# Kernel optimization log

Hardware: AMD Instinct MI355X
Metric: run time of the kernel (lower is better)

Reference implementation:

```python
import jax, jax.numpy as jnp
import numpy as np

N_QUBITS = 8
N_LAYERS = 3
B = 32768
IN_F = 512
OUT_F = 512


def _apply_1q(state, G, q):
    # state: (B, 2,...,2) complex64; G: (2,2) shared or (B,2,2) per-sample gate
    s = jnp.moveaxis(state, 1 + q, -1)
    if G.ndim == 3:
        s = jnp.einsum('bij,...j->...i'.replace('...', 'b...').replace('b...ij', 'bij'), G, s) if False else jnp.einsum('bij,b...j->b...i', G, s)
    else:
        s = jnp.einsum('ij,b...j->b...i', G, s)
    return jnp.moveaxis(s, -1, 1 + q)


def _cnot(state, c, t):
    # flip target axis on the control=1 slice
    ca, ta = 1 + c, 1 + t
    s0 = jax.lax.index_in_dim(state, 0, ca, keepdims=True)
    s1 = jax.lax.index_in_dim(state, 1, ca, keepdims=True)
    s1 = jnp.flip(s1, axis=ta)
    return jnp.concatenate([s0, s1], axis=ca)


def _circuit(angles, qparams):
    # angles: (B, 8) RY embedding angles; qparams: (3, 8) RX layer angles
    b = angles.shape[0]
    state = jnp.zeros((b, 2 ** N_QUBITS), dtype=jnp.complex64).at[:, 0].set(1.0)
    state = state.reshape((b,) + (2,) * N_QUBITS)
    # RY(theta) = [[c, -s], [s, c]], per-sample angles
    half = 0.5 * angles
    c, s = jnp.cos(half), jnp.sin(half)
    for q in range(N_QUBITS):
        G = jnp.stack([jnp.stack([c[:, q], -s[:, q]], -1),
                       jnp.stack([s[:, q], c[:, q]], -1)], -2).astype(jnp.complex64)
        state = _apply_1q(state, G, q)
    # layers: RX(params[l,q]) on each wire, then ring of CNOTs
    hp = 0.5 * qparams
    cp, sp = jnp.cos(hp), jnp.sin(hp)
    for l in range(N_LAYERS):
        for q in range(N_QUBITS):
            # RX(theta) = [[c, -i s], [-i s, c]]
            G = jnp.stack([jnp.stack([cp[l, q] + 0j, -1j * sp[l, q]], -1),
                           jnp.stack([-1j * sp[l, q], cp[l, q] + 0j], -1)], -2).astype(jnp.complex64)
            state = _apply_1q(state, G, q)
        for i in range(N_QUBITS - 1):
            state = _cnot(state, i, i + 1)
        state = _cnot(state, N_QUBITS - 1, 0)
    # <Z_q> = P(bit_q=0) - P(bit_q=1)
    probs = jnp.real(state) ** 2 + jnp.imag(state) ** 2
    zs = []
    for q in range(N_QUBITS):
        p = jnp.moveaxis(probs, 1 + q, 1).reshape(b, 2, -1).sum(-1)
        zs.append(p[:, 0] - p[:, 1])
    return jnp.stack(zs, axis=1)  # (B, 8) float32


def setup_inputs() -> dict:
    key = jax.random.key(0)
    k = jax.random.split(key, 6)
    x = jax.random.normal(k[0], (B, IN_F), dtype=jnp.float32)
    fc_w = jax.random.normal(k[1], (N_QUBITS, IN_F), dtype=jnp.float32) / np.sqrt(IN_F)
    fc_b = jax.random.normal(k[2], (N_QUBITS,), dtype=jnp.float32) * 0.01
    qparams = jax.random.normal(k[3], (N_LAYERS, N_QUBITS), dtype=jnp.float32) * 0.1
    post_w = jax.random.normal(k[4], (OUT_F, N_QUBITS), dtype=jnp.float32) / np.sqrt(N_QUBITS)
    post_b = jax.random.normal(k[5], (OUT_F,), dtype=jnp.float32) * 0.01
    return {"x": x, "fc_w": fc_w, "fc_b": fc_b, "qparams": qparams,
            "post_w": post_w, "post_b": post_b}


def reference(x, fc_w, fc_b, qparams, post_w, post_b):
    xproj = x @ fc_w.T + fc_b            # (B, 8) angles
    z = _circuit(xproj, qparams)          # (B, 8) PauliZ expectations
    return z @ post_w.T + post_b          # (B, OUT_F)
```

## Files before the change

### kernel.cpp

```cpp
#include <hip/hip_runtime.h>

#define BLOCK 512
typedef float v2f __attribute__((ext_vector_type(2)));

__device__ __forceinline__ v2f pk_fma(v2f a, v2f b, v2f c) {
  v2f d;
  asm("v_pk_fma_f32 %0, %1, %2, %3" : "=v"(d) : "v"(a), "v"(b), "v"(c));
  return d;
}
__device__ __forceinline__ v2f pk_mul(v2f a, v2f b) {
  v2f d;
  asm("v_pk_mul_f32 %0, %1, %2" : "=v"(d) : "v"(a), "v"(b));
  return d;
}
__device__ __forceinline__ v2f pk_mul_swap(v2f s, v2f p) {
  v2f d;
  asm("v_pk_mul_f32 %0, %1, %2 op_sel:[0,1] op_sel_hi:[1,0]" : "=v"(d) : "v"(s), "v"(p));
  return d;
}

template<int CTRL>
__device__ __forceinline__ float dpp_f(float v) {
  return __int_as_float(__builtin_amdgcn_mov_dpp(__float_as_int(v), CTRL, 0xF, 0xF, true));
}
template<int MASK>
__device__ __forceinline__ float shx(float v) {
  if constexpr (MASK == 1)      return dpp_f<0xB1>(v);
  else if constexpr (MASK == 2) return dpp_f<0x4E>(v);
  else if constexpr (MASK == 8) return dpp_f<0x128>(v);
  else
    return __int_as_float(__builtin_amdgcn_ds_swizzle(__float_as_int(v), 0x101F));
}

__device__ __forceinline__ int gmap(int b) {
#pragma unroll
  for (int j = 0; j < 7; ++j) b ^= ((b >> (j + 1)) & 1) << j;
  b ^= (b & 1) << 7;
  return b;
}

__device__ __forceinline__ float dotK(const v2f* pp, const v2f* kcol) {
  v2f a0; a0.x = 0.f; a0.y = 0.f;
  v2f a1; a1.x = 0.f; a1.y = 0.f;
#pragma unroll
  for (int k = 0; k < 8; k += 2) {
    a0 = pk_fma(pp[k],     kcol[k * 16],       a0);
    a1 = pk_fma(pp[k + 1], kcol[(k + 1) * 16], a1);
  }
  return (a0.x + a1.x) + (a0.y + a1.y);
}

#define MQ_PACKED 0x99CC66B359AC5632ULL

__global__ __launch_bounds__(BLOCK, 4) void qcnn_kernel(
    const float* __restrict__ x,   const float* __restrict__ fcw,
    const float* __restrict__ fcb, const float* __restrict__ qp,
    const float* __restrict__ pw,  const float* __restrict__ pb,
    float* __restrict__ out)
{
  __shared__ float s_fcw[8 * 512];
  __shared__ float s_pwt[8 * 512];
  __shared__ float s_pb[512];
  __shared__ float s_beta[256];
  __shared__ v2f   s_K2[8][8][16];

  const int tid = threadIdx.x;

#pragma unroll
  for (int i = tid; i < 1024; i += BLOCK)
    ((float4*)s_fcw)[i] = ((const float4*)fcw)[i];
#pragma unroll
  for (int i = tid; i < 4096; i += BLOCK)
    s_pwt[i] = pw[(i & 511) * 8 + (i >> 9)];
  if (tid < 128) ((float4*)s_pb)[tid] = ((const float4*)pb)[tid];

  if (tid < 256) {
    const int c = tid;
    const int i1 = gmap(c);
    const int i2 = gmap(i1);
    float ang = 0.f;
#pragma unroll
    for (int q = 0; q < 8; ++q) {
      ang += (((c  >> q) & 1) ? 0.5f : -0.5f) * qp[q];
      ang += (((i1 >> q) & 1) ? 0.5f : -0.5f) * qp[8 + q];
      ang += (((i2 >> q) & 1) ? 0.5f : -0.5f) * qp[16 + q];
    }
    s_beta[c] = ang;
  }
  __syncthreads();

#pragma unroll
  for (int i = tid; i < 2048; i += BLOCK) {
    const int q = i >> 8, c = i & 255;
    const int m = (int)((MQ_PACKED >> (8 * q)) & 0xFF);
    const float kv = __cosf(s_beta[c ^ m] - s_beta[c]) * (1.0f / 256.0f);
    const int uu = c >> 4, rr = c & 15;
    ((float*)s_K2)[((q * 8 + (rr >> 1)) * 16 + uu) * 2 + (rr & 1)] = kv;
  }
  __syncthreads();

  const int wave = tid >> 6;
  const int lane = tid & 63;
  const int u = lane & 15;
  const int g = lane >> 4;

#pragma unroll 1
  for (int tile = 0; tile < 2; ++tile) {
    const int smp = blockIdx.x * 64 + tile * 32 + wave * 4 + g;

    const float* xrow = x + (size_t)smp * 512;
    v2f acc2[8];
#pragma unroll
    for (int q = 0; q < 8; ++q) { acc2[q].x = 0.f; acc2[q].y = 0.f; }
#pragma unroll
    for (int t = 0; t < 8; ++t) {
      const float4 xv = *(const float4*)(xrow + u * 4 + t * 64);
      v2f x01; x01.x = xv.x; x01.y = xv.y;
      v2f x23; x23.x = xv.z; x23.y = xv.w;
#pragma unroll
      for (int q = 0; q < 8; ++q) {
        const float4 wv = *(const float4*)(s_fcw + q * 512 + u * 4 + t * 64);
        v2f w01; w01.x = wv.x; w01.y = wv.y;
        v2f w23; w23.x = wv.z; w23.y = wv.w;
        acc2[q] = pk_fma(x01, w01, acc2[q]);
        acc2[q] = pk_fma(x23, w23, acc2[q]);
      }
    }
    float th[8];
#pragma unroll
    for (int q = 0; q < 8; ++q) {
      float a_ = acc2[q].x + acc2[q].y;
      a_ += shx<1>(a_); a_ += shx<2>(a_); a_ += shx<4>(a_); a_ += shx<8>(a_);
      th[q] = a_ + fcb[q];
    }

    float uf[8], vf[8];
#pragma unroll
    for (int q = 0; q < 8; ++q) {
      const float h = 0.5f * th[q];
      const float c_ = __cosf(h), s_ = __sinf(h);
      uf[q] = c_ + s_; vf[q] = c_ - s_;
    }
    v2f wr2[8];
    {
      v2f P01; P01.x = uf[0]; P01.y = vf[0];
      const float r12[4] = {uf[1] * uf[2], vf[1] * uf[2], uf[1] * vf[2], vf[1] * vf[2]};
#pragma unroll
      for (int k = 0; k < 8; ++k) {
        const float rest = r12[k & 3] * ((k & 4) ? vf[3] : uf[3]);
        v2f rr; rr.x = rest; rr.y = rest;
        wr2[k] = pk_mul(P01, rr);
      }
    }
    float wup[8];
    {
      const bool b4 = (u & 1), b5 = (u & 2), b6 = (u & 4), b7 = (u & 8);
      const float f4 = b4 ? vf[4] : uf[4], g4 = b4 ? uf[4] : vf[4];
      const float f5 = b5 ? vf[5] : uf[5], g5 = b5 ? uf[5] : vf[5];
      const float f6 = b6 ? vf[6] : uf[6], g6 = b6 ? uf[6] : vf[6];
      const float f7 = b7 ? vf[7] : uf[7], g7 = b7 ? uf[7] : vf[7];
      const float A0 = f4 * f5, A1 = g4 * f5, A2 = f4 * g5, A3 = g4 * g5;
      const float B0 = f6 * f7, B1 = g6 * f7, B2 = f6 * g7, B3 = g6 * g7;
      const float wu = A0 * B0;
      wup[0] = wu * (A3 * B0);
      wup[1] = wu * (A1 * B1);
      wup[2] = wu * (A2 * B2);
      wup[3] = wup[1];
      wup[4] = wu * (A3 * B2);
      wup[5] = wu * (A2 * B1);
      wup[6] = wu * (A0 * B3);
      wup[7] = wu * (A1 * B2);
    }

    float zp[8];
    {
      const v2f* kb = (const v2f*)s_K2 + u;
      v2f pp[8];
#pragma unroll
      for (int k = 0; k < 8; ++k) pp[k] = pk_mul(wr2[k], wr2[k ^ 1]);
      zp[0] = dotK(pp, kb + 0 * 128) * wup[0];
#pragma unroll
      for (int k = 0; k < 8; ++k) pp[k] = pk_mul_swap(wr2[k], wr2[k ^ 1]);
      zp[4] = dotK(pp, kb + 4 * 128) * wup[4];
#pragma unroll
      for (int k = 0; k < 8; ++k) pp[k] = pk_mul(wr2[k], wr2[k ^ 3]);
      zp[1] = dotK(pp, kb + 1 * 128) * wup[1];
      zp[5] = dotK(pp, kb + 5 * 128) * wup[5];
#pragma unroll
      for (int k = 0; k < 8; ++k) pp[k] = pk_mul(wr2[k], wr2[k ^ 6]);
      zp[2] = dotK(pp, kb + 2 * 128) * wup[2];
      zp[6] = dotK(pp, kb + 6 * 128) * wup[6];
#pragma unroll
      for (int k = 0; k < 8; ++k) pp[k] = pk_mul_swap(wr2[k], wr2[k ^ 4]);
      zp[3] = dotK(pp, kb + 3 * 128) * wup[3];
      zp[7] = dotK(pp, kb + 7 * 128) * wup[7];
    }
#pragma unroll
    for (int q = 0; q < 8; ++q) zp[q] += shx<1>(zp[q]);
#pragma unroll
    for (int q = 0; q < 8; ++q) zp[q] += shx<2>(zp[q]);
#pragma unroll
    for (int q = 0; q < 8; ++q) zp[q] += shx<4>(zp[q]);
#pragma unroll
    for (int q = 0; q < 8; ++q) zp[q] += shx<8>(zp[q]);

    v2f zz[8];
#pragma unroll
    for (int q = 0; q < 8; ++q) { zz[q].x = zp[q]; zz[q].y = zp[q]; }
    float* orow = out + (size_t)smp * 512;
#pragma unroll
    for (int tt = 0; tt < 8; ++tt) {
      const int o = u * 4 + tt * 64;
      const float4 pbv = *(const float4*)(s_pb + o);
      v2f r0; r0.x = pbv.x; r0.y = pbv.y;
      v2f r1; r1.x = pbv.z; r1.y = pbv.w;
#pragma unroll
      for (int q = 0; q < 8; ++q) {
        const float4 wv = *(const float4*)(s_pwt + q * 512 + o);
        v2f w01; w01.x = wv.x; w01.y = wv.y;
        v2f w23; w23.x = wv.z; w23.y = wv.w;
        r0 = pk_fma(zz[q], w01, r0);
        r1 = pk_fma(zz[q], w23, r1);
      }
      float4 ov; ov.x = r0.x; ov.y = r0.y; ov.z = r1.x; ov.w = r1.y;
      *(float4*)(orow + o) = ov;
    }
  }
}

extern "C" void kernel_launch(void* const* d_in, const int* in_sizes, int n_in,
                              void* d_out, int out_size, void* d_ws, size_t ws_size,
                              hipStream_t stream) {
  const float* x   = (const float*)d_in[0];
  const float* fcw = (const float*)d_in[1];
  const float* fcb = (const float*)d_in[2];
  const float* qp  = (const float*)d_in[3];
  const float* pw  = (const float*)d_in[4];
  const float* pb  = (const float*)d_in[5];
  float* out = (float*)d_out;

  dim3 grid(512), block(BLOCK);
  hipLaunchKernelGGL(qcnn_kernel, grid, block, 0, stream, x, fcw, fcb, qp, pw, pb, out);
}
```

Measured before the change: 134.5 us.

## Process two samples per thread group concurrently to share LDS weight loads

Replaces the sequential two-tile loop with one pass in which each 16-lane group handles two samples (A and B) at once. Every LDS read of fc weights, K2 kernel entries and post weights now feeds two samples, which halves LDS traffic per sample and exposes more independent instructions for latency hiding. Both samples' global x loads are also issued together. The cost is roughly doubled register pressure, which under launch_bounds(512,4) could cause spills or limit occupancy.

```diff
diff --git a/kernel.cpp b/kernel.cpp
--- a/kernel.cpp
+++ b/kernel.cpp
@@ -39,18 +39,41 @@
   return b;
 }
 
-__device__ __forceinline__ float dotK(const v2f* pp, const v2f* kcol) {
-  v2f a0; a0.x = 0.f; a0.y = 0.f;
-  v2f a1; a1.x = 0.f; a1.y = 0.f;
-#pragma unroll
-  for (int k = 0; k < 8; k += 2) {
-    a0 = pk_fma(pp[k],     kcol[k * 16],       a0);
-    a1 = pk_fma(pp[k + 1], kcol[(k + 1) * 16], a1);
-  }
-  return (a0.x + a1.x) + (a0.y + a1.y);
-}
-
 #define MQ_PACKED 0x99CC66B359AC5632ULL
+
+__device__ __forceinline__ void build_w(const float* th, int u, v2f* wr2, float* wup) {
+  float uf[8], vf[8];
+#pragma unroll
+  for (int q = 0; q < 8; ++q) {
+    const float h = 0.5f * th[q];
+    const float c_ = __cosf(h), s_ = __sinf(h);
+    uf[q] = c_ + s_; vf[q] = c_ - s_;
+  }
+  v2f P01; P01.x = uf[0]; P01.y = vf[0];
+  const float r12[4] = {uf[1] * uf[2], vf[1] * uf[2], uf[1] * vf[2], vf[1] * vf[2]};
+#pragma unroll
+  for (int k = 0; k < 8; ++k) {
+    const float rest = r12[k & 3] * ((k & 4) ? vf[3] : uf[3]);
+    v2f rr; rr.x = rest; rr.y = rest;
+    wr2[k] = pk_mul(P01, rr);
+  }
+  const bool b4 = (u & 1), b5 = (u & 2), b6 = (u & 4), b7 = (u & 8);
+  const float f4 = b4 ? vf[4] : uf[4], g4 = b4 ? uf[4] : vf[4];
+  const float f5 = b5 ? vf[5] : uf[5], g5 = b5 ? uf[5] : vf[5];
+  const float f6 = b6 ? vf[6] : uf[6], g6 = b6 ? uf[6] : vf[6];
+  const float f7 = b7 ? vf[7] : uf[7], g7 = b7 ? uf[7] : vf[7];
+  const float A0 = f4 * f5, A1 = g4 * f5, A2 = f4 * g5, A3 = g4 * g5;
+  const float B0 = f6 * f7, B1 = g6 * f7, B2 = f6 * g7, B3 = g6 * g7;
+  const float wu = A0 * B0;
+  wup[0] = wu * (A3 * B0);
+  wup[1] = wu * (A1 * B1);
+  wup[2] = wu * (A2 * B2);
+  wup[3] = wup[1];
+  wup[4] = wu * (A3 * B2);
+  wup[5] = wu * (A2 * B1);
+  wup[6] = wu * (A0 * B3);
+  wup[7] = wu * (A1 * B2);
+}
 
 __global__ __launch_bounds__(BLOCK, 4) void qcnn_kernel(
     const float* __restrict__ x,   const float* __restrict__ fcw,
@@ -104,127 +127,167 @@
   const int u = lane & 15;
   const int g = lane >> 4;
 
-#pragma unroll 1
-  for (int tile = 0; tile < 2; ++tile) {
-    const int smp = blockIdx.x * 64 + tile * 32 + wave * 4 + g;
-
-    const float* xrow = x + (size_t)smp * 512;
-    v2f acc2[8];
-#pragma unroll
-    for (int q = 0; q < 8; ++q) { acc2[q].x = 0.f; acc2[q].y = 0.f; }
-#pragma unroll
-    for (int t = 0; t < 8; ++t) {
-      const float4 xv = *(const float4*)(xrow + u * 4 + t * 64);
-      v2f x01; x01.x = xv.x; x01.y = xv.y;
-      v2f x23; x23.x = xv.z; x23.y = xv.w;
-#pragma unroll
-      for (int q = 0; q < 8; ++q) {
-        const float4 wv = *(const float4*)(s_fcw + q * 512 + u * 4 + t * 64);
-        v2f w01; w01.x = wv.x; w01.y = wv.y;
-        v2f w23; w23.x = wv.z; w23.y = wv.w;
-        acc2[q] = pk_fma(x01, w01, acc2[q]);
-        acc2[q] = pk_fma(x23, w23, acc2[q]);
-      }
-    }
-    float th[8];
+  const int base = blockIdx.x * 64 + wave * 8;
+  const int sA = base + g;
+  const int sB = base + 4 + g;
+
+  const float* xrA = x + (size_t)sA * 512;
+  const float* xrB = x + (size_t)sB * 512;
+  v2f accA[8], accB[8];
+#pragma unroll
+  for (int q = 0; q < 8; ++q) {
+    accA[q].x = 0.f; accA[q].y = 0.f;
+    accB[q].x = 0.f; accB[q].y = 0.f;
+  }
+#pragma unroll
+  for (int t = 0; t < 8; ++t) {
+    const float4 xa = *(const float4*)(xrA + u * 4 + t * 64);
+    const float4 xb = *(const float4*)(xrB + u * 4 + t * 64);
+    v2f xa01; xa01.x = xa.x; xa01.y = xa.y;
+    v2f xa23; xa23.x = xa.z; xa23.y = xa.w;
+    v2f xb01; xb01.x = xb.x; xb01.y = xb.y;
+    v2f xb23; xb23.x = xb.z; xb23.y = xb.w;
 #pragma unroll
     for (int q = 0; q < 8; ++q) {
-      float a_ = acc2[q].x + acc2[q].y;
-      a_ += shx<1>(a_); a_ += shx<2>(a_); a_ += shx<4>(a_); a_ += shx<8>(a_);
-      th[q] = a_ + fcb[q];
-    }
-
-    float uf[8], vf[8];
+      const float4 wv = *(const float4*)(s_fcw + q * 512 + u * 4 + t * 64);
+      v2f w01; w01.x = wv.x; w01.y = wv.y;
+      v2f w23; w23.x = wv.z; w23.y = wv.w;
+      accA[q] = pk_fma(xa01, w01, accA[q]);
+      accA[q] = pk_fma(xa23, w23, accA[q]);
+      accB[q] = pk_fma(xb01, w01, accB[q]);
+      accB[q] = pk_fma(xb23, w23, accB[q]);
+    }
+  }
+  float thA[8], thB[8];
+#pragma unroll
+  for (int q = 0; q < 8; ++q) {
+    float aA = accA[q].x + accA[q].y;
+    float aB = accB[q].x + accB[q].y;
+    aA += shx<1>(aA); aB += shx<1>(aB);
+    aA += shx<2>(aA); aB += shx<2>(aB);
+    aA += shx<4>(aA); aB += shx<4>(aB);
+    aA += shx<8>(aA); aB += shx<8>(aB);
+    const float fb = fcb[q];
+    thA[q] = aA + fb; thB[q] = aB + fb;
+  }
+
+  v2f wA[8], wB[8];
+  float wupA[8], wupB[8];
+  build_w(thA, u, wA, wupA);
+  build_w(thB, u, wB, wupB);
+
+  float zpA[8], zpB[8];
+  {
+    const v2f* kb = (const v2f*)s_K2 + u;
+    {
+      v2f aA; aA.x = 0.f; aA.y = 0.f; v2f aB = aA;
+#pragma unroll
+      for (int k = 0; k < 8; ++k) {
+        const v2f kv = kb[0 * 128 + k * 16];
+        aA = pk_fma(pk_mul(wA[k], wA[k ^ 1]), kv, aA);
+        aB = pk_fma(pk_mul(wB[k], wB[k ^ 1]), kv, aB);
+      }
+      zpA[0] = (aA.x + aA.y) * wupA[0];
+      zpB[0] = (aB.x + aB.y) * wupB[0];
+    }
+    {
+      v2f aA; aA.x = 0.f; aA.y = 0.f; v2f aB = aA;
+#pragma unroll
+      for (int k = 0; k < 8; ++k) {
+        const v2f kv = kb[4 * 128 + k * 16];
+        aA = pk_fma(pk_mul_swap(wA[k], wA[k ^ 1]), kv, aA);
+        aB = pk_fma(pk_mul_swap(wB[k], wB[k ^ 1]), kv, aB);
+      }
+      zpA[4] = (aA.x + aA.y) * wupA[4];
+      zpB[4] = (aB.x + aB.y) * wupB[4];
+    }
+    {
+      v2f a1A, a5A, a1B, a5B;
+      a1A.x = a1A.y = a5A.x = a5A.y = 0.f;
+      a1B.x = a1B.y = a5B.x = a5B.y = 0.f;
+#pragma unroll
+      for (int k = 0; k < 8; ++k) {
+        const v2f k1 = kb[1 * 128 + k * 16];
+        const v2f k5 = kb[5 * 128 + k * 16];
+        const v2f pA = pk_mul(wA[k], wA[k ^ 3]);
+        const v2f pB = pk_mul(wB[k], wB[k ^ 3]);
+        a1A = pk_fma(pA, k1, a1A); a5A = pk_fma(pA, k5, a5A);
+        a1B = pk_fma(pB, k1, a1B); a5B = pk_fma(pB, k5, a5B);
+      }
+      zpA[1] = (a1A.x + a1A.y) * wupA[1]; zpA[5] = (a5A.x + a5A.y) * wupA[5];
+      zpB[1] = (a1B.x + a1B.y) * wupB[1]; zpB[5] = (a5B.x + a5B.y) * wupB[5];
+    }
+    {
+      v2f a2A, a6A, a2B, a6B;
+      a2A.x = a2A.y = a6A.x = a6A.y = 0.f;
+      a2B.x = a2B.y = a6B.x = a6B.y = 0.f;
+#pragma unroll
+      for (int k = 0; k < 8; ++k) {
+        const v2f k2 = kb[2 * 128 + k * 16];
+        const v2f k6 = kb[6 * 128 + k * 16];
+        const v2f pA = pk_mul(wA[k], wA[k ^ 6]);
+        const v2f pB = pk_mul(wB[k], wB[k ^ 6]);
+        a2A = pk_fma(pA, k2, a2A); a6A = pk_fma(pA, k6, a6A);
+        a2B = pk_fma(pB, k2, a2B); a6B = pk_fma(pB, k6, a6B);
+      }
+      zpA[2] = (a2A.x + a2A.y) * wupA[2]; zpA[6] = (a6A.x + a6A.y) * wupA[6];
+      zpB[2] = (a2B.x + a2B.y) * wupB[2]; zpB[6] = (a6B.x + a6B.y) * wupB[6];
+    }
+    {
+      v2f a3A, a7A, a3B, a7B;
+      a3A.x = a3A.y = a7A.x = a7A.y = 0.f;
+      a3B.x = a3B.y = a7B.x = a7B.y = 0.f;
+#pragma unroll
+      for (int k = 0; k < 8; ++k) {
+        const v2f k3 = kb[3 * 128 + k * 16];
+        const v2f k7 = kb[7 * 128 + k * 16];
+        const v2f pA = pk_mul_swap(wA[k], wA[k ^ 4]);
+        const v2f pB = pk_mul_swap(wB[k], wB[k ^ 4]);
+        a3A = pk_fma(pA, k3, a3A); a7A = pk_fma(pA, k7, a7A);
+        a3B = pk_fma(pB, k3, a3B); a7B = pk_fma(pB, k7, a7B);
+      }
+      zpA[3] = (a3A.x + a3A.y) * wupA[3]; zpA[7] = (a7A.x + a7A.y) * wupA[7];
+      zpB[3] = (a3B.x + a3B.y) * wupB[3]; zpB[7] = (a7B.x + a7B.y) * wupB[7];
+    }
+  }
+#pragma unroll
+  for (int q = 0; q < 8; ++q) { zpA[q] += shx<1>(zpA[q]); zpB[q] += shx<1>(zpB[q]); }
+#pragma unroll
+  for (int q = 0; q < 8; ++q) { zpA[q] += shx<2>(zpA[q]); zpB[q] += shx<2>(zpB[q]); }
+#pragma unroll
+  for (int q = 0; q < 8; ++q) { zpA[q] += shx<4>(zpA[q]); zpB[q] += shx<4>(zpB[q]); }
+#pragma unroll
+  for (int q = 0; q < 8; ++q) { zpA[q] += shx<8>(zpA[q]); zpB[q] += shx<8>(zpB[q]); }
+
+  v2f zzA[8], zzB[8];
+#pragma unroll
+  for (int q = 0; q < 8; ++q) {
+    zzA[q].x = zpA[q]; zzA[q].y = zpA[q];
+    zzB[q].x = zpB[q]; zzB[q].y = zpB[q];
+  }
+  float* orA = out + (size_t)sA * 512;
+  float* orB = out + (size_t)sB * 512;
+#pragma unroll
+  for (int tt = 0; tt < 8; ++tt) {
+    const int o = u * 4 + tt * 64;
+    const float4 pbv = *(const float4*)(s_pb + o);
+    v2f rA0; rA0.x = pbv.x; rA0.y = pbv.y;
+    v2f rA1; rA1.x = pbv.z; rA1.y = pbv.w;
+    v2f rB0 = rA0, rB1 = rA1;
 #pragma unroll
     for (int q = 0; q < 8; ++q) {
-      const float h = 0.5f * th[q];
-      const float c_ = __cosf(h), s_ = __sinf(h);
-      uf[q] = c_ + s_; vf[q] = c_ - s_;
-    }
-    v2f wr2[8];
-    {
-      v2f P01; P01.x = uf[0]; P01.y = vf[0];
-      const float r12[4] = {uf[1] * uf[2], vf[1] * uf[2], uf[1] * vf[2], vf[1] * vf[2]};
-#pragma unroll
-      for (int k = 0; k < 8; ++k) {
-        const float rest = r12[k & 3] * ((k & 4) ? vf[3] : uf[3]);
-        v2f rr; rr.x = rest; rr.y = rest;
-        wr2[k] = pk_mul(P01, rr);
-      }
-    }
-    float wup[8];
-    {
-      const bool b4 = (u & 1), b5 = (u & 2), b6 = (u & 4), b7 = (u & 8);
-      const float f4 = b4 ? vf[4] : uf[4], g4 = b4 ? uf[4] : vf[4];
-      const float f5 = b5 ? vf[5] : uf[5], g5 = b5 ? uf[5] : vf[5];
-      const float f6 = b6 ? vf[6] : uf[6], g6 = b6 ? uf[6] : vf[6];
-      const float f7 = b7 ? vf[7] : uf[7], g7 = b7 ? uf[7] : vf[7];
-      const float A0 = f4 * f5, A1 = g4 * f5, A2 = f4 * g5, A3 = g4 * g5;
-      const float B0 = f6 * f7, B1 = g6 * f7, B2 = f6 * g7, B3 = g6 * g7;
-      const float wu = A0 * B0;
-      wup[0] = wu * (A3 * B0);
-      wup[1] = wu * (A1 * B1);
-      wup[2] = wu * (A2 * B2);
-      wup[3] = wup[1];
-      wup[4] = wu * (A3 * B2);
-      wup[5] = wu * (A2 * B1);
-      wup[6] = wu * (A0 * B3);
-      wup[7] = wu * (A1 * B2);
-    }
-
-    float zp[8];
-    {
-      const v2f* kb = (const v2f*)s_K2 + u;
-      v2f pp[8];
-#pragma unroll
-      for (int k = 0; k < 8; ++k) pp[k] = pk_mul(wr2[k], wr2[k ^ 1]);
-      zp[0] = dotK(pp, kb + 0 * 128) * wup[0];
-#pragma unroll
-      for (int k = 0; k < 8; ++k) pp[k] = pk_mul_swap(wr2[k], wr2[k ^ 1]);
-      zp[4] = dotK(pp, kb + 4 * 128) * wup[4];
-#pragma unroll
-      for (int k = 0; k < 8; ++k) pp[k] = pk_mul(wr2[k], wr2[k ^ 3]);
-      zp[1] = dotK(pp, kb + 1 * 128) * wup[1];
-      zp[5] = dotK(pp, kb + 5 * 128) * wup[5];
-#pragma unroll
-      for (int k = 0; k < 8; ++k) pp[k] = pk_mul(wr2[k], wr2[k ^ 6]);
-      zp[2] = dotK(pp, kb + 2 * 128) * wup[2];
-      zp[6] = dotK(pp, kb + 6 * 128) * wup[6];
-#pragma unroll
-      for (int k = 0; k < 8; ++k) pp[k] = pk_mul_swap(wr2[k], wr2[k ^ 4]);
-      zp[3] = dotK(pp, kb + 3 * 128) * wup[3];
-      zp[7] = dotK(pp, kb + 7 * 128) * wup[7];
-    }
-#pragma unroll
-    for (int q = 0; q < 8; ++q) zp[q] += shx<1>(zp[q]);
-#pragma unroll
-    for (int q = 0; q < 8; ++q) zp[q] += shx<2>(zp[q]);
-#pragma unroll
-    for (int q = 0; q < 8; ++q) zp[q] += shx<4>(zp[q]);
-#pragma unroll
-    for (int q = 0; q < 8; ++q) zp[q] += shx<8>(zp[q]);
-
-    v2f zz[8];
-#pragma unroll
-    for (int q = 0; q < 8; ++q) { zz[q].x = zp[q]; zz[q].y = zp[q]; }
-    float* orow = out + (size_t)smp * 512;
-#pragma unroll
-    for (int tt = 0; tt < 8; ++tt) {
-      const int o = u * 4 + tt * 64;
-      const float4 pbv = *(const float4*)(s_pb + o);
-      v2f r0; r0.x = pbv.x; r0.y = pbv.y;
-      v2f r1; r1.x = pbv.z; r1.y = pbv.w;
-#pragma unroll
-      for (int q = 0; q < 8; ++q) {
-        const float4 wv = *(const float4*)(s_pwt + q * 512 + o);
-        v2f w01; w01.x = wv.x; w01.y = wv.y;
-        v2f w23; w23.x = wv.z; w23.y = wv.w;
-        r0 = pk_fma(zz[q], w01, r0);
-        r1 = pk_fma(zz[q], w23, r1);
-      }
-      float4 ov; ov.x = r0.x; ov.y = r0.y; ov.z = r1.x; ov.w = r1.y;
-      *(float4*)(orow + o) = ov;
-    }
+      const float4 wv = *(const float4*)(s_pwt + q * 512 + o);
+      v2f w01; w01.x = wv.x; w01.y = wv.y;
+      v2f w23; w23.x = wv.z; w23.y = wv.w;
+      rA0 = pk_fma(zzA[q], w01, rA0);
+      rA1 = pk_fma(zzA[q], w23, rA1);
+      rB0 = pk_fma(zzB[q], w01, rB0);
+      rB1 = pk_fma(zzB[q], w23, rB1);
+    }
+    float4 ovA; ovA.x = rA0.x; ovA.y = rA0.y; ovA.z = rA1.x; ovA.w = rA1.y;
+    float4 ovB; ovB.x = rB0.x; ovB.y = rB0.y; ovB.z = rB1.x; ovB.w = rB1.y;
+    *(float4*)(orA + o) = ovA;
+    *(float4*)(orB + o) = ovB;
   }
 }
 
```

Measured after the change: 124.6 us. -7.3%, faster.

## Process four samples per wave group with register blocking and early x prefetch

Applied to the files above, without the earlier changes.

Each wave now handles 16 samples at once, four per lane group, instead of looping over two tiles of four. This lets each shared-memory weight and K-matrix load serve four samples. All x rows are prefetched into registers before the shared-memory setup so global loads overlap the prologue, and the K table is re-laid out for float4 reads. The pw transpose load is vectorised and outputs are written with nontemporal stores. The grid is halved and launch bounds lowered to 2, which trades occupancy for heavy register pressure (128 x floats per thread plus accumulators) and risks spills.

```diff
diff --git a/kernel.cpp b/kernel.cpp
--- a/kernel.cpp
+++ b/kernel.cpp
@@ -2,6 +2,7 @@
 
 #define BLOCK 512
 typedef float v2f __attribute__((ext_vector_type(2)));
+typedef float v4f __attribute__((ext_vector_type(4)));
 
 __device__ __forceinline__ v2f pk_fma(v2f a, v2f b, v2f c) {
   v2f d;
@@ -39,20 +40,99 @@
   return b;
 }
 
-__device__ __forceinline__ float dotK(const v2f* pp, const v2f* kcol) {
-  v2f a0; a0.x = 0.f; a0.y = 0.f;
-  v2f a1; a1.x = 0.f; a1.y = 0.f;
-#pragma unroll
-  for (int k = 0; k < 8; k += 2) {
-    a0 = pk_fma(pp[k],     kcol[k * 16],       a0);
-    a1 = pk_fma(pp[k + 1], kcol[(k + 1) * 16], a1);
-  }
-  return (a0.x + a1.x) + (a0.y + a1.y);
-}
-
 #define MQ_PACKED 0x99CC66B359AC5632ULL
 
-__global__ __launch_bounds__(BLOCK, 4) void qcnn_kernel(
+__device__ __forceinline__ void build_w(const float* th, int u, v2f* wr2, float* wup) {
+  float uf[8], vf[8];
+#pragma unroll
+  for (int q = 0; q < 8; ++q) {
+    const float h = 0.5f * th[q];
+    const float c_ = __cosf(h), s_ = __sinf(h);
+    uf[q] = c_ + s_; vf[q] = c_ - s_;
+  }
+  v2f P01; P01.x = uf[0]; P01.y = vf[0];
+  const float r12[4] = {uf[1] * uf[2], vf[1] * uf[2], uf[1] * vf[2], vf[1] * vf[2]};
+#pragma unroll
+  for (int k = 0; k < 8; ++k) {
+    const float rest = r12[k & 3] * ((k & 4) ? vf[3] : uf[3]);
+    v2f rr; rr.x = rest; rr.y = rest;
+    wr2[k] = pk_mul(P01, rr);
+  }
+  const bool b4 = (u & 1), b5 = (u & 2), b6 = (u & 4), b7 = (u & 8);
+  const float f4 = b4 ? vf[4] : uf[4], g4 = b4 ? uf[4] : vf[4];
+  const float f5 = b5 ? vf[5] : uf[5], g5 = b5 ? uf[5] : vf[5];
+  const float f6 = b6 ? vf[6] : uf[6], g6 = b6 ? uf[6] : vf[6];
+  const float f7 = b7 ? vf[7] : uf[7], g7 = b7 ? uf[7] : vf[7];
+  const float A0 = f4 * f5, A1 = g4 * f5, A2 = f4 * g5, A3 = g4 * g5;
+  const float B0 = f6 * f7, B1 = g6 * f7, B2 = f6 * g7, B3 = g6 * g7;
+  const float wu = A0 * B0;
+  wup[0] = wu * (A3 * B0);
+  wup[1] = wu * (A1 * B1);
+  wup[2] = wu * (A2 * B2);
+  wup[3] = wup[1];
+  wup[4] = wu * (A3 * B2);
+  wup[5] = wu * (A2 * B1);
+  wup[6] = wu * (A0 * B3);
+  wup[7] = wu * (A1 * B2);
+}
+
+template<int Q, int XOR, bool SWAP>
+__device__ __forceinline__ void dot1r(const float4* kb4, const v2f (&w)[4][8],
+                                      const float (&wup)[4][8], float (&zp)[4][8]) {
+  v2f a[4];
+#pragma unroll
+  for (int r = 0; r < 4; ++r) { a[r].x = 0.f; a[r].y = 0.f; }
+#pragma unroll
+  for (int k2 = 0; k2 < 4; ++k2) {
+    const float4 kv = kb4[(Q * 4 + k2) * 16];
+    v2f klo; klo.x = kv.x; klo.y = kv.y;
+    v2f khi; khi.x = kv.z; khi.y = kv.w;
+    const int k0 = 2 * k2, k1 = 2 * k2 + 1;
+#pragma unroll
+    for (int r = 0; r < 4; ++r) {
+      v2f p0 = SWAP ? pk_mul_swap(w[r][k0], w[r][k0 ^ XOR]) : pk_mul(w[r][k0], w[r][k0 ^ XOR]);
+      v2f p1 = SWAP ? pk_mul_swap(w[r][k1], w[r][k1 ^ XOR]) : pk_mul(w[r][k1], w[r][k1 ^ XOR]);
+      a[r] = pk_fma(p0, klo, a[r]);
+      a[r] = pk_fma(p1, khi, a[r]);
+    }
+  }
+#pragma unroll
+  for (int r = 0; r < 4; ++r) zp[r][Q] = (a[r].x + a[r].y) * wup[r][Q];
+}
+template<int Q1, int Q2, int XOR, bool SWAP>
+__device__ __forceinline__ void dot2r(const float4* kb4, const v2f (&w)[4][8],
+                                      const float (&wup)[4][8], float (&zp)[4][8]) {
+  v2f a1[4], a2[4];
+#pragma unroll
+  for (int r = 0; r < 4; ++r) {
+    a1[r].x = a1[r].y = 0.f;
+    a2[r].x = a2[r].y = 0.f;
+  }
+#pragma unroll
+  for (int k2 = 0; k2 < 4; ++k2) {
+    const float4 kv1 = kb4[(Q1 * 4 + k2) * 16];
+    const float4 kv2 = kb4[(Q2 * 4 + k2) * 16];
+    v2f k1lo; k1lo.x = kv1.x; k1lo.y = kv1.y;
+    v2f k1hi; k1hi.x = kv1.z; k1hi.y = kv1.w;
+    v2f k2lo; k2lo.x = kv2.x; k2lo.y = kv2.y;
+    v2f k2hi; k2hi.x = kv2.z; k2hi.y = kv2.w;
+    const int k0 = 2 * k2, k1 = 2 * k2 + 1;
+#pragma unroll
+    for (int r = 0; r < 4; ++r) {
+      v2f p0 = SWAP ? pk_mul_swap(w[r][k0], w[r][k0 ^ XOR]) : pk_mul(w[r][k0], w[r][k0 ^ XOR]);
+      v2f p1 = SWAP ? pk_mul_swap(w[r][k1], w[r][k1 ^ XOR]) : pk_mul(w[r][k1], w[r][k1 ^ XOR]);
+      a1[r] = pk_fma(p0, k1lo, a1[r]); a1[r] = pk_fma(p1, k1hi, a1[r]);
+      a2[r] = pk_fma(p0, k2lo, a2[r]); a2[r] = pk_fma(p1, k2hi, a2[r]);
+    }
+  }
+#pragma unroll
+  for (int r = 0; r < 4; ++r) {
+    zp[r][Q1] = (a1[r].x + a1[r].y) * wup[r][Q1];
+    zp[r][Q2] = (a2[r].x + a2[r].y) * wup[r][Q2];
+  }
+}
+
+__global__ __launch_bounds__(BLOCK, 2) void qcnn_kernel(
     const float* __restrict__ x,   const float* __restrict__ fcw,
     const float* __restrict__ fcb, const float* __restrict__ qp,
     const float* __restrict__ pw,  const float* __restrict__ pb,
@@ -62,18 +142,35 @@
   __shared__ float s_pwt[8 * 512];
   __shared__ float s_pb[512];
   __shared__ float s_beta[256];
-  __shared__ v2f   s_K2[8][8][16];
+  __shared__ float s_K3[8][4][16][4];
 
   const int tid = threadIdx.x;
-
-#pragma unroll
+  const int wave = tid >> 6;
+  const int lane = tid & 63;
+  const int u = lane & 15;
+  const int g = lane >> 4;
+
+  const int base = blockIdx.x * 128 + wave * 16;
+
+  float4 xp[4][8];
+#pragma unroll
+  for (int r = 0; r < 4; ++r) {
+    const float* xr = x + (size_t)(base + r * 4 + g) * 512 + u * 4;
+#pragma unroll
+    for (int t = 0; t < 8; ++t) xp[r][t] = *(const float4*)(xr + t * 64);
+  }
+
   for (int i = tid; i < 1024; i += BLOCK)
     ((float4*)s_fcw)[i] = ((const float4*)fcw)[i];
-#pragma unroll
-  for (int i = tid; i < 4096; i += BLOCK)
-    s_pwt[i] = pw[(i & 511) * 8 + (i >> 9)];
+  for (int i = tid; i < 1024; i += BLOCK) {
+    const float4 v = ((const float4*)pw)[i];
+    const int row = i >> 1, c0 = 4 * (i & 1);
+    s_pwt[(c0 + 0) * 512 + row] = v.x;
+    s_pwt[(c0 + 1) * 512 + row] = v.y;
+    s_pwt[(c0 + 2) * 512 + row] = v.z;
+    s_pwt[(c0 + 3) * 512 + row] = v.w;
+  }
   if (tid < 128) ((float4*)s_pb)[tid] = ((const float4*)pb)[tid];
-
   if (tid < 256) {
     const int c = tid;
     const int i1 = gmap(c);
@@ -89,141 +186,118 @@
   }
   __syncthreads();
 
-#pragma unroll
   for (int i = tid; i < 2048; i += BLOCK) {
     const int q = i >> 8, c = i & 255;
     const int m = (int)((MQ_PACKED >> (8 * q)) & 0xFF);
     const float kv = __cosf(s_beta[c ^ m] - s_beta[c]) * (1.0f / 256.0f);
-    const int uu = c >> 4, rr = c & 15;
-    ((float*)s_K2)[((q * 8 + (rr >> 1)) * 16 + uu) * 2 + (rr & 1)] = kv;
+    s_K3[q][(c & 15) >> 2][c >> 4][c & 3] = kv;
   }
   __syncthreads();
 
-  const int wave = tid >> 6;
-  const int lane = tid & 63;
-  const int u = lane & 15;
-  const int g = lane >> 4;
-
-#pragma unroll 1
-  for (int tile = 0; tile < 2; ++tile) {
-    const int smp = blockIdx.x * 64 + tile * 32 + wave * 4 + g;
-
-    const float* xrow = x + (size_t)smp * 512;
-    v2f acc2[8];
-#pragma unroll
-    for (int q = 0; q < 8; ++q) { acc2[q].x = 0.f; acc2[q].y = 0.f; }
-#pragma unroll
-    for (int t = 0; t < 8; ++t) {
-      const float4 xv = *(const float4*)(xrow + u * 4 + t * 64);
-      v2f x01; x01.x = xv.x; x01.y = xv.y;
-      v2f x23; x23.x = xv.z; x23.y = xv.w;
-#pragma unroll
-      for (int q = 0; q < 8; ++q) {
-        const float4 wv = *(const float4*)(s_fcw + q * 512 + u * 4 + t * 64);
-        v2f w01; w01.x = wv.x; w01.y = wv.y;
-        v2f w23; w23.x = wv.z; w23.y = wv.w;
-        acc2[q] = pk_fma(x01, w01, acc2[q]);
-        acc2[q] = pk_fma(x23, w23, acc2[q]);
+  v2f acc[4][8];
+#pragma unroll
+  for (int r = 0; r < 4; ++r)
+#pragma unroll
+    for (int q = 0; q < 8; ++q) { acc[r][q].x = 0.f; acc[r][q].y = 0.f; }
+#pragma unroll
+  for (int t = 0; t < 8; ++t) {
+    v2f x01[4], x23[4];
+#pragma unroll
+    for (int r = 0; r < 4; ++r) {
+      x01[r].x = xp[r][t].x; x01[r].y = xp[r][t].y;
+      x23[r].x = xp[r][t].z; x23[r].y = xp[r][t].w;
+    }
+#pragma unroll
+    for (int q = 0; q < 8; ++q) {
+      const float4 wv = *(const float4*)(s_fcw + q * 512 + u * 4 + t * 64);
+      v2f w01; w01.x = wv.x; w01.y = wv.y;
+      v2f w23; w23.x = wv.z; w23.y = wv.w;
+#pragma unroll
+      for (int r = 0; r < 4; ++r) {
+        acc[r][q] = pk_fma(x01[r], w01, acc[r][q]);
+        acc[r][q] = pk_fma(x23[r], w23, acc[r][q]);
       }
     }
-    float th[8];
+  }
+  float th[4][8];
+#pragma unroll
+  for (int q = 0; q < 8; ++q) {
+    const float fb = fcb[q];
+#pragma unroll
+    for (int r = 0; r < 4; ++r) {
+      float a_ = acc[r][q].x + acc[r][q].y;
+      a_ += shx<1>(a_);
+      a_ += shx<2>(a_);
+      a_ += shx<4>(a_);
+      a_ += shx<8>(a_);
+      th[r][q] = a_ + fb;
+    }
+  }
+
+  v2f w4[4][8];
+  float wup4[4][8];
+#pragma unroll
+  for (int r = 0; r < 4; ++r) build_w(th[r], u, w4[r], wup4[r]);
+
+  float zp[4][8];
+  {
+    const float4* kb4 = ((const float4*)s_K3) + u;
+    dot1r<0, 1, false>(kb4, w4, wup4, zp);
+    dot1r<4, 1, true >(kb4, w4, wup4, zp);
+    dot2r<1, 5, 3, false>(kb4, w4, wup4, zp);
+    dot2r<2, 6, 6, false>(kb4, w4, wup4, zp);
+    dot2r<3, 7, 4, true >(kb4, w4, wup4, zp);
+  }
+#pragma unroll
+  for (int q = 0; q < 8; ++q)
+#pragma unroll
+    for (int r = 0; r < 4; ++r) zp[r][q] += shx<1>(zp[r][q]);
+#pragma unroll
+  for (int q = 0; q < 8; ++q)
+#pragma unroll
+    for (int r = 0; r < 4; ++r) zp[r][q] += shx<2>(zp[r][q]);
+#pragma unroll
+  for (int q = 0; q < 8; ++q)
+#pragma unroll
+    for (int r = 0; r < 4; ++r) zp[r][q] += shx<4>(zp[r][q]);
+#pragma unroll
+  for (int q = 0; q < 8; ++q)
+#pragma unroll
+    for (int r = 0; r < 4; ++r) zp[r][q] += shx<8>(zp[r][q]);
+
+  v2f zz[4][8];
+#pragma unroll
+  for (int r = 0; r < 4; ++r)
+#pragma unroll
+    for (int q = 0; q < 8; ++q) { zz[r][q].x = zp[r][q]; zz[r][q].y = zp[r][q]; }
+  float* orp[4];
+#pragma unroll
+  for (int r = 0; r < 4; ++r) orp[r] = out + (size_t)(base + r * 4 + g) * 512;
+#pragma unroll
+  for (int tt = 0; tt < 8; ++tt) {
+    const int o = u * 4 + tt * 64;
+    const float4 pbv = *(const float4*)(s_pb + o);
+    v2f r0[4], r1[4];
+#pragma unroll
+    for (int r = 0; r < 4; ++r) {
+      r0[r].x = pbv.x; r0[r].y = pbv.y;
+      r1[r].x = pbv.z; r1[r].y = pbv.w;
+    }
 #pragma unroll
     for (int q = 0; q < 8; ++q) {
-      float a_ = acc2[q].x + acc2[q].y;
-      a_ += shx<1>(a_); a_ += shx<2>(a_); a_ += shx<4>(a_); a_ += shx<8>(a_);
-      th[q] = a_ + fcb[q];
-    }
-
-    float uf[8], vf[8];
-#pragma unroll
-    for (int q = 0; q < 8; ++q) {
-      const float h = 0.5f * th[q];
-      const float c_ = __cosf(h), s_ = __sinf(h);
-      uf[q] = c_ + s_; vf[q] = c_ - s_;
-    }
-    v2f wr2[8];
-    {
-      v2f P01; P01.x = uf[0]; P01.y = vf[0];
-      const float r12[4] = {uf[1] * uf[2], vf[1] * uf[2], uf[1] * vf[2], vf[1] * vf[2]};
-#pragma unroll
-      for (int k = 0; k < 8; ++k) {
-        const float rest = r12[k & 3] * ((k & 4) ? vf[3] : uf[3]);
-        v2f rr; rr.x = rest; rr.y = rest;
-        wr2[k] = pk_mul(P01, rr);
+      const float4 wv = *(const float4*)(s_pwt + q * 512 + o);
+      v2f w01; w01.x = wv.x; w01.y = wv.y;
+      v2f w23; w23.x = wv.z; w23.y = wv.w;
+#pragma unroll
+      for (int r = 0; r < 4; ++r) {
+        r0[r] = pk_fma(zz[r][q], w01, r0[r]);
+        r1[r] = pk_fma(zz[r][q], w23, r1[r]);
       }
     }
-    float wup[8];
-    {
-      const bool b4 = (u & 1), b5 = (u & 2), b6 = (u & 4), b7 = (u & 8);
-      const float f4 = b4 ? vf[4] : uf[4], g4 = b4 ? uf[4] : vf[4];
-      const float f5 = b5 ? vf[5] : uf[5], g5 = b5 ? uf[5] : vf[5];
-      const float f6 = b6 ? vf[6] : uf[6], g6 = b6 ? uf[6] : vf[6];
-      const float f7 = b7 ? vf[7] : uf[7], g7 = b7 ? uf[7] : vf[7];
-      const float A0 = f4 * f5, A1 = g4 * f5, A2 = f4 * g5, A3 = g4 * g5;
-      const float B0 = f6 * f7, B1 = g6 * f7, B2 = f6 * g7, B3 = g6 * g7;
-      const float wu = A0 * B0;
-      wup[0] = wu * (A3 * B0);
-      wup[1] = wu * (A1 * B1);
-      wup[2] = wu * (A2 * B2);
-      wup[3] = wup[1];
-      wup[4] = wu * (A3 * B2);
-      wup[5] = wu * (A2 * B1);
-      wup[6] = wu * (A0 * B3);
-      wup[7] = wu * (A1 * B2);
-    }
-
-    float zp[8];
-    {
-      const v2f* kb = (const v2f*)s_K2 + u;
-      v2f pp[8];
-#pragma unroll
-      for (int k = 0; k < 8; ++k) pp[k] = pk_mul(wr2[k], wr2[k ^ 1]);
-      zp[0] = dotK(pp, kb + 0 * 128) * wup[0];
-#pragma unroll
-      for (int k = 0; k < 8; ++k) pp[k] = pk_mul_swap(wr2[k], wr2[k ^ 1]);
-      zp[4] = dotK(pp, kb + 4 * 128) * wup[4];
-#pragma unroll
-      for (int k = 0; k < 8; ++k) pp[k] = pk_mul(wr2[k], wr2[k ^ 3]);
-      zp[1] = dotK(pp, kb + 1 * 128) * wup[1];
-      zp[5] = dotK(pp, kb + 5 * 128) * wup[5];
-#pragma unroll
-      for (int k = 0; k < 8; ++k) pp[k] = pk_mul(wr2[k], wr2[k ^ 6]);
-      zp[2] = dotK(pp, kb + 2 * 128) * wup[2];
-      zp[6] = dotK(pp, kb + 6 * 128) * wup[6];
-#pragma unroll
-      for (int k = 0; k < 8; ++k) pp[k] = pk_mul_swap(wr2[k], wr2[k ^ 4]);
-      zp[3] = dotK(pp, kb + 3 * 128) * wup[3];
-      zp[7] = dotK(pp, kb + 7 * 128) * wup[7];
-    }
-#pragma unroll
-    for (int q = 0; q < 8; ++q) zp[q] += shx<1>(zp[q]);
-#pragma unroll
-    for (int q = 0; q < 8; ++q) zp[q] += shx<2>(zp[q]);
-#pragma unroll
-    for (int q = 0; q < 8; ++q) zp[q] += shx<4>(zp[q]);
-#pragma unroll
-    for (int q = 0; q < 8; ++q) zp[q] += shx<8>(zp[q]);
-
-    v2f zz[8];
-#pragma unroll
-    for (int q = 0; q < 8; ++q) { zz[q].x = zp[q]; zz[q].y = zp[q]; }
-    float* orow = out + (size_t)smp * 512;
-#pragma unroll
-    for (int tt = 0; tt < 8; ++tt) {
-      const int o = u * 4 + tt * 64;
-      const float4 pbv = *(const float4*)(s_pb + o);
-      v2f r0; r0.x = pbv.x; r0.y = pbv.y;
-      v2f r1; r1.x = pbv.z; r1.y = pbv.w;
-#pragma unroll
-      for (int q = 0; q < 8; ++q) {
-        const float4 wv = *(const float4*)(s_pwt + q * 512 + o);
-        v2f w01; w01.x = wv.x; w01.y = wv.y;
-        v2f w23; w23.x = wv.z; w23.y = wv.w;
-        r0 = pk_fma(zz[q], w01, r0);
-        r1 = pk_fma(zz[q], w23, r1);
-      }
-      float4 ov; ov.x = r0.x; ov.y = r0.y; ov.z = r1.x; ov.w = r1.y;
-      *(float4*)(orow + o) = ov;
+#pragma unroll
+    for (int r = 0; r < 4; ++r) {
+      v4f ov; ov.x = r0[r].x; ov.y = r0[r].y; ov.z = r1[r].x; ov.w = r1[r].y;
+      __builtin_nontemporal_store(ov, (v4f*)(orp[r] + o));
     }
   }
 }
@@ -239,6 +313,6 @@
   const float* pb  = (const float*)d_in[5];
   float* out = (float*)d_out;
 
-  dim3 grid(512), block(BLOCK);
+  dim3 grid(256), block(BLOCK);
   hipLaunchKernelGGL(qcnn_kernel, grid, block, 0, stream, x, fcw, fcb, qp, pw, pb, out);
 }
```

After: 123.7 us. -8.0%, faster.
